# Performance work log

Hardware: AMD Instinct MI355X
Metric: run time of the kernel (lower is better)

Reference implementation:

```python
import jax, jax.numpy as jnp
import numpy as np


def _conv(x, w, b, padding='SAME' if False else 'VALID'):
    # NCHW conv, OIHW weights
    out = jax.lax.conv_general_dilated(
        x, w, window_strides=(1, 1), padding=padding,
        dimension_numbers=('NCHW', 'OIHW', 'NCHW'))
    return out + b[None, :, None, None]


def setup_inputs() -> dict:
    key = jax.random.key(0)
    ks = jax.random.split(key, 14)
    s = lambda k, shape, scale=0.1: jax.random.normal(k, shape, dtype=jnp.float32) * scale
    return {
        'x': jax.random.normal(ks[0], (8, 16, 512, 512), dtype=jnp.float32),
        'y': jax.random.normal(ks[1], (8, 5, 512, 512), dtype=jnp.float32),
        'fuse_w': s(ks[2], (16, 5, 1, 1)),
        'fuse_b': s(ks[3], (16,)),
        'se_w1': s(ks[4], (16, 16)),
        'se_w2': s(ks[5], (5, 16)),
        'bd_w': s(ks[6], (2, 5, 1, 1)),
        'bd_b': s(ks[7], (2,)),
        'fc_w': s(ks[8], (16, 32, 3, 3)),
        'fc_b': s(ks[9], (16,)),
        'fm_w': s(ks[10], (2, 16, 1, 1)),
        'fm_b': s(ks[11], (2,)),
        'cv_w': s(ks[12], (16, 1, 1, 1)),
        'cv_b': s(ks[13], (16,)),
    }


def reference(x, y, fuse_w, fuse_b, se_w1, se_w2, bd_w, bd_b,
              fc_w, fc_b, fm_w, fm_b, cv_w, cv_b):
    # fuse: 1x1 conv 5->16 + ReLU
    fuse_box = jax.nn.relu(_conv(y, fuse_w, fuse_b, 'VALID'))  # [B,16,H,W]
    # global average pool -> SE mimic MLP -> sigmoid gate over 5 channels
    gap = jnp.mean(fuse_box, axis=(2, 3))                       # [B,16]
    se = jax.nn.sigmoid(jax.nn.relu(gap @ se_w1.T) @ se_w2.T)   # [B,5]
    feat_se = y * se[:, :, None, None]                          # [B,5,H,W]
    # boundary head: 1x1 conv 5->2, softmax over channel, take fg prob
    boundary = _conv(feat_se, bd_w, bd_b, 'VALID')              # [B,2,H,W]
    boundary_scale = jax.nn.softmax(boundary, axis=1)[:, 1:2]   # [B,1,H,W]
    # mask head: concat(x, fuse_box) -> 3x3 conv 32->16 + ReLU -> 1x1 conv 16->2
    feat_concat = jnp.concatenate([x, fuse_box], axis=1)        # [B,32,H,W]
    fcc = jax.nn.relu(_conv(feat_concat, fc_w, fc_b, 'SAME'))   # [B,16,H,W]
    mask = _conv(fcc, fm_w, fm_b, 'VALID')                      # [B,2,H,W]
    mask_scale = jax.nn.softmax(mask, axis=1)[:, 1:2]           # [B,1,H,W]
    # fused scale factor, clamp, expand to 16 channels via 1x1 conv
    scalefactor = jnp.clip(mask_scale + boundary_scale, 0.0, 1.0)
    return _conv(scalefactor, cv_w, cv_b, 'VALID')              # [B,16,H,W]
```

## Files before the change

### kernel.cpp

```cpp
#include <hip/hip_runtime.h>
#include <hip/hip_bf16.h>

#define HW 262144
#define IW 512
#define TW 64
#define TH 8
#define HLW 66
#define HLH 10
#define NHALO (HLW*HLH)
#define ROWU 40

typedef __attribute__((ext_vector_type(8))) short short8;
typedef __attribute__((ext_vector_type(4))) float f32x4;
typedef __attribute__((ext_vector_type(4))) unsigned int uint4v;

static __device__ inline unsigned int bpack2(float a, float b) {
  __hip_bfloat16 ha = __float2bfloat16(a);
  __hip_bfloat16 hb = __float2bfloat16(b);
  unsigned short ua = *reinterpret_cast<unsigned short*>(&ha);
  unsigned short ub = *reinterpret_cast<unsigned short*>(&hb);
  return (unsigned int)ua | ((unsigned int)ub << 16);
}

__global__ __launch_bounds__(256) void k_gap(
    const float* __restrict__ y, const float* __restrict__ fuse_w,
    const float* __restrict__ fuse_b, float* __restrict__ partial) {
  __shared__ float fw[80], fb[16];
  __shared__ float red[4][16];
  int tid = threadIdx.x;
  if (tid < 80) fw[tid] = fuse_w[tid];
  if (tid < 16) fb[tid] = fuse_b[tid];
  __syncthreads();

  int b = blockIdx.x >> 7;
  int chunk = blockIdx.x & 127;
  const float* yb = y + (size_t)b * 5 * HW + chunk * 2048;

  float sums[16];
#pragma unroll
  for (int o = 0; o < 16; ++o) sums[o] = 0.f;

  for (int i = 0; i < 2048; i += 256) {
    int p = i + tid;
    float yv[5];
#pragma unroll
    for (int c = 0; c < 5; ++c) yv[c] = yb[c * HW + p];
#pragma unroll
    for (int o = 0; o < 16; ++o) {
      float a = fb[o];
#pragma unroll
      for (int c = 0; c < 5; ++c) a = fmaf(fw[o * 5 + c], yv[c], a);
      sums[o] += fmaxf(a, 0.f);
    }
  }

  int lane = tid & 63, wv = tid >> 6;
#pragma unroll
  for (int o = 0; o < 16; ++o) {
    float v = sums[o];
    for (int off = 32; off > 0; off >>= 1) v += __shfl_down(v, off);
    if (lane == 0) red[wv][o] = v;
  }
  __syncthreads();
  if (tid < 16)
    partial[blockIdx.x * 16 + tid] =
        red[0][tid] + red[1][tid] + red[2][tid] + red[3][tid];
}

__global__ __launch_bounds__(256) void k_se(
    const float* __restrict__ partial, const float* __restrict__ se_w1,
    const float* __restrict__ se_w2, const float* __restrict__ bd_w,
    float* __restrict__ bd_eff) {
  int tid = threadIdx.x;
  int b = tid >> 5, sub = tid & 31;
  float g[16];
#pragma unroll
  for (int c = 0; c < 16; ++c) g[c] = 0.f;
#pragma unroll
  for (int k = 0; k < 4; ++k) {
    const float* p = partial + (b * 128 + sub + k * 32) * 16;
#pragma unroll
    for (int c = 0; c < 16; ++c) g[c] += p[c];
  }
#pragma unroll
  for (int c = 0; c < 16; ++c) {
    float v = g[c];
    v += __shfl_xor(v, 1);  v += __shfl_xor(v, 2);
    v += __shfl_xor(v, 4);  v += __shfl_xor(v, 8);
    v += __shfl_xor(v, 16);
    g[c] = v * (1.f / 262144.f);
  }
  if (sub == 0) {
    float h[16];
#pragma unroll
    for (int j = 0; j < 16; ++j) {
      float s = 0.f;
#pragma unroll
      for (int c = 0; c < 16; ++c) s += g[c] * se_w1[j * 16 + c];
      h[j] = fmaxf(s, 0.f);
    }
#pragma unroll
    for (int i = 0; i < 5; ++i) {
      float s = 0.f;
#pragma unroll
      for (int j = 0; j < 16; ++j) s += h[j] * se_w2[i * 16 + j];
      float se = 1.f / (1.f + expf(-s));
      bd_eff[b * 10 + i]     = bd_w[i] * se;
      bd_eff[b * 10 + 5 + i] = bd_w[5 + i] * se;
    }
  }
}

__global__ void k_prep(const float* __restrict__ fc_w,
                       unsigned short* __restrict__ wTab) {
  int i = blockIdx.x * 256 + threadIdx.x;
  if (i < 4608) {
    int ci = i & 31, rest = i >> 5;
    int oc = rest & 15, s = rest >> 4;
    float v = fc_w[(oc * 32 + ci) * 9 + s];
    __hip_bfloat16 h = __float2bfloat16(v);
    wTab[i] = *reinterpret_cast<unsigned short*>(&h);
  }
}

__global__ __launch_bounds__(256) void k_main(
    const float* __restrict__ x, const float* __restrict__ y,
    const float* __restrict__ fuse_w, const float* __restrict__ fuse_b,
    const unsigned short* __restrict__ wTab,
    const float* __restrict__ bd_eff, const float* __restrict__ bd_b,
    const float* __restrict__ fc_b,
    const float* __restrict__ fm_w, const float* __restrict__ fm_b,
    const float* __restrict__ cv_w, const float* __restrict__ cv_b,
    float* __restrict__ out) {
  __shared__ unsigned short tile[NHALO * ROWU];
  __shared__ float s_fw[80], s_fb[16], s_bde[10], s_bdb[2], s_fm[32],
      s_fmb[2], s_cv[16], s_cvb[16], s_fcb[16];

  int tid = threadIdx.x;
  int bsel = blockIdx.z;
  int h0 = blockIdx.y * TH;
  int w0 = blockIdx.x * TW;

  if (tid < 80) s_fw[tid] = fuse_w[tid];
  else if (tid < 96)  s_fb[tid - 80]   = fuse_b[tid - 80];
  else if (tid < 106) s_bde[tid - 96]  = bd_eff[bsel * 10 + tid - 96];
  else if (tid < 108) s_bdb[tid - 106] = bd_b[tid - 106];
  else if (tid < 140) s_fm[tid - 108]  = fm_w[tid - 108];
  else if (tid < 142) s_fmb[tid - 140] = fm_b[tid - 140];
  else if (tid < 158) s_cv[tid - 142]  = cv_w[tid - 142];
  else if (tid < 174) s_cvb[tid - 158] = cv_b[tid - 158];
  else if (tid < 190) s_fcb[tid - 174] = fc_b[tid - 174];

  int lane = tid & 63, wv = tid >> 6;
  int l15 = lane & 15, q = lane >> 4;

  short8 afrag[9];
#pragma unroll
  for (int s = 0; s < 9; ++s)
    afrag[s] = *reinterpret_cast<const short8*>(wTab + (s * 16 + l15) * 32 + q * 8);

  __syncthreads();

  const float* yb = y + (size_t)bsel * 5 * HW;
  const float* xb = x + (size_t)bsel * 16 * HW;
  for (int p = tid; p < NHALO; p += 256) {
    int hr = p / HLW, wc = p - hr * HLW;
    int gh = h0 - 1 + hr, gw = w0 - 1 + wc;
    bool valid = (gh >= 0) & (gh < IW) & (gw >= 0) & (gw < IW);
    uint4v blk0 = {0, 0, 0, 0}, blk1 = {0, 0, 0, 0},
           blk2 = {0, 0, 0, 0}, blk3 = {0, 0, 0, 0};
    if (valid) {
      int gofs = gh * IW + gw;
      float xv[16], yv[5];
#pragma unroll
      for (int c = 0; c < 16; ++c) xv[c] = xb[c * HW + gofs];
#pragma unroll
      for (int c = 0; c < 5; ++c) yv[c] = yb[c * HW + gofs];
      float fo[16];
#pragma unroll
      for (int o = 0; o < 16; ++o) {
        float a = s_fb[o];
#pragma unroll
        for (int c = 0; c < 5; ++c) a = fmaf(s_fw[o * 5 + c], yv[c], a);
        fo[o] = fmaxf(a, 0.f);
      }
      blk0 = uint4v{bpack2(xv[0], xv[1]), bpack2(xv[2], xv[3]),
                    bpack2(xv[4], xv[5]), bpack2(xv[6], xv[7])};
      blk1 = uint4v{bpack2(xv[8], xv[9]), bpack2(xv[10], xv[11]),
                    bpack2(xv[12], xv[13]), bpack2(xv[14], xv[15])};
      blk2 = uint4v{bpack2(fo[0], fo[1]), bpack2(fo[2], fo[3]),
                    bpack2(fo[4], fo[5]), bpack2(fo[6], fo[7])};
      blk3 = uint4v{bpack2(fo[8], fo[9]), bpack2(fo[10], fo[11]),
                    bpack2(fo[12], fo[13]), bpack2(fo[14], fo[15])};
    }
    uint4v* dst = reinterpret_cast<uint4v*>(&tile[p * ROWU]);
    dst[0] = blk0; dst[1] = blk1; dst[2] = blk2; dst[3] = blk3;
  }
  __syncthreads();

  const float* outb0 = nullptr; (void)outb0;
  float* outb = out + (size_t)bsel * 16 * HW;
  const char* tbase = reinterpret_cast<const char*>(tile);

#pragma unroll 1
  for (int g = 0; g < 8; ++g) {
    int row = 2 * wv + (g >> 2);
    int c0 = (g & 3) * 16;
    int hp0 = row * HLW + c0 + l15;
    const char* bp = tbase + hp0 * (ROWU * 2) + q * 16;

    f32x4 acc = {0.f, 0.f, 0.f, 0.f};
#pragma unroll
    for (int kh = 0; kh < 3; ++kh) {
#pragma unroll
      for (int kw = 0; kw < 3; ++kw) {
        short8 bfr = *reinterpret_cast<const short8*>(
            bp + (kh * HLW + kw) * (ROWU * 2));
        acc = __builtin_amdgcn_mfma_f32_16x16x32_bf16(afrag[kh * 3 + kw], bfr,
                                                      acc, 0, 0, 0);
      }
    }

    float pm0 = 0.f, pm1 = 0.f;
#pragma unroll
    for (int j = 0; j < 4; ++j) {
      int oc = q * 4 + j;
      float fv = fmaxf(acc[j] + s_fcb[oc], 0.f);
      pm0 = fmaf(s_fm[oc], fv, pm0);
      pm1 = fmaf(s_fm[16 + oc], fv, pm1);
    }
    pm0 += __shfl_xor(pm0, 16); pm0 += __shfl_xor(pm0, 32);
    pm1 += __shfl_xor(pm1, 16); pm1 += __shfl_xor(pm1, 32);
    float m0 = pm0 + s_fmb[0], m1 = pm1 + s_fmb[1];
    float mscale = 1.f / (1.f + __expf(m0 - m1));

    int gh = h0 + row, gw = w0 + c0 + l15;
    int gofs = gh * IW + gw;
    float bl0 = s_bdb[0], bl1 = s_bdb[1];
#pragma unroll
    for (int c = 0; c < 5; ++c) {
      float yv = yb[c * HW + gofs];
      bl0 = fmaf(s_bde[c], yv, bl0);
      bl1 = fmaf(s_bde[5 + c], yv, bl1);
    }
    float bscale = 1.f / (1.f + __expf(bl0 - bl1));
    float sc = fminf(fmaxf(mscale + bscale, 0.f), 1.f);
#pragma unroll
    for (int j = 0; j < 4; ++j) {
      int oc = q * 4 + j;
      outb[oc * HW + gofs] = fmaf(s_cv[oc], sc, s_cvb[oc]);
    }
  }
}

extern "C" void kernel_launch(void* const* d_in, const int* in_sizes, int n_in,
                              void* d_out, int out_size, void* d_ws, size_t ws_size,
                              hipStream_t stream) {
  const float* x      = (const float*)d_in[0];
  const float* y      = (const float*)d_in[1];
  const float* fuse_w = (const float*)d_in[2];
  const float* fuse_b = (const float*)d_in[3];
  const float* se_w1  = (const float*)d_in[4];
  const float* se_w2  = (const float*)d_in[5];
  const float* bd_w   = (const float*)d_in[6];
  const float* bd_b   = (const float*)d_in[7];
  const float* fc_w   = (const float*)d_in[8];
  const float* fc_b   = (const float*)d_in[9];
  const float* fm_w   = (const float*)d_in[10];
  const float* fm_b   = (const float*)d_in[11];
  const float* cv_w   = (const float*)d_in[12];
  const float* cv_b   = (const float*)d_in[13];
  float* out = (float*)d_out;

  float* partial = (float*)d_ws;
  float* bd_eff  = partial + 1024 * 16;
  unsigned short* wTab =
      (unsigned short*)((char*)d_ws + (1024 * 16 + 80) * 4);

  k_gap<<<1024, 256, 0, stream>>>(y, fuse_w, fuse_b, partial);
  k_se<<<1, 256, 0, stream>>>(partial, se_w1, se_w2, bd_w, bd_eff);
  k_prep<<<18, 256, 0, stream>>>(fc_w, wTab);
  k_main<<<dim3(8, 64, 8), 256, 0, stream>>>(x, y, fuse_w, fuse_b, wTab,
                                             bd_eff, bd_b, fc_b, fm_w, fm_b,
                                             cv_w, cv_b, out);
}
```

Measured before the change: 139.0 us.

## Use 512-thread blocks, cache boundary scale in LDS, vectorize output stores

The boundary-scale softmax is now computed during halo loading from the y values already in registers and stored in the tile's padding slots. This removes the second global read of y in the epilogue. Blocks grow to 512 threads, with each wave handling one row of four 16-pixel groups. The per-pixel scale factors are staged in LDS so the 16-channel output can be written with coalesced float4 stores. In exchange, register pressure rises from the 512,4 launch bounds and there is an extra barrier.

New measurement: 369.5 us. 2.66x slower.

```diff
diff --git a/kernel.cpp b/kernel.cpp
--- a/kernel.cpp
+++ b/kernel.cpp
@@ -6,8 +6,7 @@
 #define TW 64
 #define TH 8
 #define HLW 66
-#define HLH 10
-#define NHALO (HLW*HLH)
+#define NHALO 660
 #define ROWU 40
 
 typedef __attribute__((ext_vector_type(8))) short short8;
@@ -123,7 +122,7 @@
   }
 }
 
-__global__ __launch_bounds__(256) void k_main(
+__global__ __launch_bounds__(512, 4) void k_main(
     const float* __restrict__ x, const float* __restrict__ y,
     const float* __restrict__ fuse_w, const float* __restrict__ fuse_b,
     const unsigned short* __restrict__ wTab,
@@ -133,6 +132,7 @@
     const float* __restrict__ cv_w, const float* __restrict__ cv_b,
     float* __restrict__ out) {
   __shared__ unsigned short tile[NHALO * ROWU];
+  __shared__ float scbuf[512];
   __shared__ float s_fw[80], s_fb[16], s_bde[10], s_bdb[2], s_fm[32],
       s_fmb[2], s_cv[16], s_cvb[16], s_fcb[16];
 
@@ -163,12 +163,13 @@
 
   const float* yb = y + (size_t)bsel * 5 * HW;
   const float* xb = x + (size_t)bsel * 16 * HW;
-  for (int p = tid; p < NHALO; p += 256) {
+  for (int p = tid; p < NHALO; p += 512) {
     int hr = p / HLW, wc = p - hr * HLW;
     int gh = h0 - 1 + hr, gw = w0 - 1 + wc;
     bool valid = (gh >= 0) & (gh < IW) & (gw >= 0) & (gw < IW);
     uint4v blk0 = {0, 0, 0, 0}, blk1 = {0, 0, 0, 0},
            blk2 = {0, 0, 0, 0}, blk3 = {0, 0, 0, 0};
+    float bsc = 0.f;
     if (valid) {
       int gofs = gh * IW + gw;
       float xv[16], yv[5];
@@ -184,6 +185,13 @@
         for (int c = 0; c < 5; ++c) a = fmaf(s_fw[o * 5 + c], yv[c], a);
         fo[o] = fmaxf(a, 0.f);
       }
+      float bl0 = s_bdb[0], bl1 = s_bdb[1];
+#pragma unroll
+      for (int c = 0; c < 5; ++c) {
+        bl0 = fmaf(s_bde[c], yv[c], bl0);
+        bl1 = fmaf(s_bde[5 + c], yv[c], bl1);
+      }
+      bsc = 1.f / (1.f + __expf(bl0 - bl1));
       blk0 = uint4v{bpack2(xv[0], xv[1]), bpack2(xv[2], xv[3]),
                     bpack2(xv[4], xv[5]), bpack2(xv[6], xv[7])};
       blk1 = uint4v{bpack2(xv[8], xv[9]), bpack2(xv[10], xv[11]),
@@ -195,17 +203,16 @@
     }
     uint4v* dst = reinterpret_cast<uint4v*>(&tile[p * ROWU]);
     dst[0] = blk0; dst[1] = blk1; dst[2] = blk2; dst[3] = blk3;
-  }
-  __syncthreads();
-
-  const float* outb0 = nullptr; (void)outb0;
-  float* outb = out + (size_t)bsel * 16 * HW;
+    *reinterpret_cast<float*>(&tile[p * ROWU + 32]) = bsc;
+  }
+  __syncthreads();
+
   const char* tbase = reinterpret_cast<const char*>(tile);
-
-#pragma unroll 1
-  for (int g = 0; g < 8; ++g) {
-    int row = 2 * wv + (g >> 2);
-    int c0 = (g & 3) * 16;
+  int row = wv;
+  float scv[4];
+#pragma unroll
+  for (int g = 0; g < 4; ++g) {
+    int c0 = g * 16;
     int hp0 = row * HLW + c0 + l15;
     const char* bp = tbase + hp0 * (ROWU * 2) + q * 16;
 
@@ -231,25 +238,30 @@
     }
     pm0 += __shfl_xor(pm0, 16); pm0 += __shfl_xor(pm0, 32);
     pm1 += __shfl_xor(pm1, 16); pm1 += __shfl_xor(pm1, 32);
-    float m0 = pm0 + s_fmb[0], m1 = pm1 + s_fmb[1];
-    float mscale = 1.f / (1.f + __expf(m0 - m1));
-
-    int gh = h0 + row, gw = w0 + c0 + l15;
-    int gofs = gh * IW + gw;
-    float bl0 = s_bdb[0], bl1 = s_bdb[1];
-#pragma unroll
-    for (int c = 0; c < 5; ++c) {
-      float yv = yb[c * HW + gofs];
-      bl0 = fmaf(s_bde[c], yv, bl0);
-      bl1 = fmaf(s_bde[5 + c], yv, bl1);
-    }
-    float bscale = 1.f / (1.f + __expf(bl0 - bl1));
-    float sc = fminf(fmaxf(mscale + bscale, 0.f), 1.f);
-#pragma unroll
-    for (int j = 0; j < 4; ++j) {
-      int oc = q * 4 + j;
-      outb[oc * HW + gofs] = fmaf(s_cv[oc], sc, s_cvb[oc]);
-    }
+    float mscale = 1.f / (1.f + __expf((pm0 + s_fmb[0]) - (pm1 + s_fmb[1])));
+    float bsc = *reinterpret_cast<const float*>(
+        tbase + ((row + 1) * HLW + c0 + l15 + 1) * (ROWU * 2) + 64);
+    scv[g] = fminf(fmaxf(mscale + bsc, 0.f), 1.f);
+  }
+
+  if (q == 0) {
+#pragma unroll
+    for (int g = 0; g < 4; ++g) scbuf[wv * 64 + g * 16 + l15] = scv[g];
+  }
+  __syncthreads();
+
+  float* outb = out + (size_t)bsel * 16 * HW;
+#pragma unroll
+  for (int it = 0; it < 4; ++it) {
+    int t = tid + it * 512;
+    int oc = t >> 7, grp = t & 127;
+    int p = grp * 4, prow = p >> 6, pcol = p & 63;
+    f32x4 sv = *reinterpret_cast<const f32x4*>(&scbuf[p]);
+    float cw = s_cv[oc], cb = s_cvb[oc];
+    f32x4 ov = {fmaf(cw, sv[0], cb), fmaf(cw, sv[1], cb),
+                fmaf(cw, sv[2], cb), fmaf(cw, sv[3], cb)};
+    *reinterpret_cast<f32x4*>(
+        &outb[(size_t)oc * HW + (h0 + prow) * IW + w0 + pcol]) = ov;
   }
 }
 
@@ -280,7 +292,7 @@
   k_gap<<<1024, 256, 0, stream>>>(y, fuse_w, fuse_b, partial);
   k_se<<<1, 256, 0, stream>>>(partial, se_w1, se_w2, bd_w, bd_eff);
   k_prep<<<18, 256, 0, stream>>>(fc_w, wTab);
-  k_main<<<dim3(8, 64, 8), 256, 0, stream>>>(x, y, fuse_w, fuse_b, wTab,
+  k_main<<<dim3(8, 64, 8), 512, 0, stream>>>(x, y, fuse_w, fuse_b, wTab,
                                              bd_eff, bd_b, fc_b, fm_w, fm_b,
                                              cv_w, cv_b, out);
 }
```
